# Optimization experiments

Hardware: AMD Instinct MI355X
Metric: run time of the kernel (lower is better)

The kernel has to match this reference:

```python
import jax, jax.numpy as jnp
import numpy as np

FEAT_SIZE, HIDDEN_SIZE, ATT_SIZE = 2048, 1024, 512
BATCH, FEAT_NUM = 64, 512


def setup_inputs() -> dict:
    key = jax.random.key(0)
    ks = jax.random.split(key, 8)
    s = lambda fan_in: 1.0 / np.sqrt(fan_in)
    return {
        "feats": jax.random.normal(ks[0], (BATCH, FEAT_NUM, FEAT_SIZE), jnp.float32),
        "key": jax.random.normal(ks[1], (BATCH, HIDDEN_SIZE), jnp.float32),
        "wh_w": jax.random.uniform(ks[2], (ATT_SIZE, HIDDEN_SIZE), jnp.float32, -s(HIDDEN_SIZE), s(HIDDEN_SIZE)),
        "wh_b": jax.random.uniform(ks[3], (ATT_SIZE,), jnp.float32, -s(HIDDEN_SIZE), s(HIDDEN_SIZE)),
        "wv_w": jax.random.uniform(ks[4], (ATT_SIZE, FEAT_SIZE), jnp.float32, -s(FEAT_SIZE), s(FEAT_SIZE)),
        "wv_b": jax.random.uniform(ks[5], (ATT_SIZE,), jnp.float32, -s(FEAT_SIZE), s(FEAT_SIZE)),
        "wa_w": jax.random.uniform(ks[6], (1, ATT_SIZE), jnp.float32, -s(ATT_SIZE), s(ATT_SIZE)),
    }


def reference(feats, key, wh_w, wh_b, wv_w, wv_b, wa_w):
    # v = wv(feats): (B, N, A)
    v = jnp.einsum('bnf,af->bna', feats, wv_w) + wv_b
    # h = wh(key): (B, A), broadcast-added over feat_num
    h = key @ wh_w.T + wh_b
    inputs = h[:, None, :] + v                       # (B, N, A)
    scores = jnp.einsum('bna,a->bn', jnp.tanh(inputs), wa_w[0])  # (B, N)
    alpha = jax.nn.softmax(scores, axis=1)           # (B, N)
    att_feats = jnp.einsum('bn,bnf->bf', alpha, feats)  # (B, F)
    return (att_feats, alpha)
```

## Files before the change

### kernel.cpp

```cpp
#include <hip/hip_runtime.h>
#include <hip/hip_bf16.h>

#define FEATSZ 2048
#define HIDSZ  1024
#define ATTSZ  512
#define BATCH  64
#define FEATN  512

typedef float  f32x4  __attribute__((ext_vector_type(4)));
typedef __bf16 bf16x8 __attribute__((ext_vector_type(8)));

__device__ __forceinline__ unsigned short f2bf(float f) {
    union { float f; unsigned int u; } x; x.f = f;
    unsigned int u = x.u;
    return (unsigned short)((u + 0x7fffu + ((u >> 16) & 1u)) >> 16);
}

__global__ void k_h(const float* __restrict__ key, const float* __restrict__ wh_w,
                    const float* __restrict__ wh_b, float* __restrict__ h) {
    const int b = blockIdx.y;
    const int ac = blockIdx.x;
    const int t = threadIdx.x;
    const int lane = t & 63, wv = t >> 6;
    float k16[16];
    const float* kb = key + b * HIDSZ;
#pragma unroll
    for (int j = 0; j < 16; ++j) k16[j] = kb[lane + 64 * j];
#pragma unroll 1
    for (int i = 0; i < 16; ++i) {
        int a = ac * 64 + wv * 16 + i;
        const float* wr = wh_w + (size_t)a * HIDSZ;
        float s = 0.f;
#pragma unroll
        for (int j = 0; j < 16; ++j) s += k16[j] * wr[lane + 64 * j];
#pragma unroll
        for (int d = 32; d; d >>= 1) s += __shfl_xor(s, d);
        if (lane == 0) h[b * ATTSZ + a] = s + wh_b[a];
    }
}

__global__ void k_wvcvt(const float* __restrict__ wv_w, unsigned short* __restrict__ wvb) {
    int idx = blockIdx.x * 256 + threadIdx.x;
    int a = idx >> 11, k = idx & 2047;
    int CF = a >> 4, c = a & 15, ks = k >> 5, kin = k & 31;
    int lane = c + ((kin >> 3) << 4);
    int dst = ((ks * 32 + CF) * 64 + lane) * 8 + (kin & 7);
    wvb[dst] = f2bf(wv_w[idx]);
}

__global__ __launch_bounds__(512) void k_scores(
        const float* __restrict__ feats, const unsigned short* __restrict__ wvb,
        const float* __restrict__ h, const float* __restrict__ wv_b,
        const float* __restrict__ wa, float* __restrict__ scores) {
    __shared__ __align__(16) char Abuf[4][8192];
    __shared__ float scp[8][128];
    const int t = threadIdx.x, lane = t & 63, w = t >> 6;
    const int m0 = blockIdx.x * 128, b = blockIdx.x >> 2;

    const int srow = t >> 2, sq = t & 3;
    const float* gsrc = feats + (size_t)(m0 + srow) * FEATSZ + sq * 8;
    const int wboff = srow * 64 + ((sq ^ ((t >> 3) & 3)) * 16);

    const int rbase = (lane & 15) * 64 + (((lane >> 4) ^ ((lane >> 1) & 3)) * 16);

    const unsigned short* wb = wvb + (size_t)(w * 4) * 512 + lane * 8;

    f32x4 acc[8][4];
#pragma unroll
    for (int m = 0; m < 8; ++m)
#pragma unroll
        for (int cf = 0; cf < 4; ++cf) acc[m][cf] = (f32x4)0.0f;

    f32x4 GA0, GA1, GB0, GB1;
    bf16x8 BX[4], BY[4];

    auto loadBX = [&](int tile) {
#pragma unroll
        for (int cf = 0; cf < 4; ++cf) BX[cf] = *(const bf16x8*)(wb + (size_t)(tile * 32 + cf) * 512);
    };
    auto loadBY = [&](int tile) {
#pragma unroll
        for (int cf = 0; cf < 4; ++cf) BY[cf] = *(const bf16x8*)(wb + (size_t)(tile * 32 + cf) * 512);
    };
    auto writeA = [&](f32x4 r0, f32x4 r1, int tile) {
        bf16x8 v;
        v[0] = (__bf16)r0[0]; v[1] = (__bf16)r0[1]; v[2] = (__bf16)r0[2]; v[3] = (__bf16)r0[3];
        v[4] = (__bf16)r1[0]; v[5] = (__bf16)r1[1]; v[6] = (__bf16)r1[2]; v[7] = (__bf16)r1[3];
        *(bf16x8*)__builtin_assume_aligned(&Abuf[tile & 3][0] + wboff, 16) = v;
    };
    auto bar = [&]() {
        asm volatile("s_waitcnt lgkmcnt(0)" ::: "memory");
        __builtin_amdgcn_s_barrier();
        __builtin_amdgcn_sched_barrier(0);
    };

    {
        const float* p0 = gsrc;
        GA0 = *(const f32x4*)p0;        GA1 = *(const f32x4*)(p0 + 4);
        const float* p1 = gsrc + 32;
        GB0 = *(const f32x4*)p1;        GB1 = *(const f32x4*)(p1 + 4);
        loadBX(0);
        writeA(GA0, GA1, 0);
        bar();
    }

#pragma unroll 1
    for (int jj = 0; jj < 32; ++jj) {
        const int j = jj * 2;
        if (j <= 61) {
            const float* p = gsrc + (j + 2) * 32;
            GA0 = *(const f32x4*)p; GA1 = *(const f32x4*)(p + 4);
        }
        loadBY(j + 1);
        writeA(GB0, GB1, j + 1);
        {
            const char* ab = &Abuf[j & 3][0];
            __builtin_amdgcn_s_setprio(1);
#pragma unroll
            for (int m = 0; m < 8; ++m) {
                bf16x8 a = *(const bf16x8*)__builtin_assume_aligned(ab + m * 1024 + rbase, 16);
#pragma unroll
                for (int cf = 0; cf < 4; ++cf)
                    acc[m][cf] = __builtin_amdgcn_mfma_f32_16x16x32_bf16(a, BX[cf], acc[m][cf], 0, 0, 0);
            }
            __builtin_amdgcn_s_setprio(0);
        }
        bar();
        const int j1 = j + 1;
        if (j1 <= 61) {
            const float* p = gsrc + (j1 + 2) * 32;
            GB0 = *(const f32x4*)p; GB1 = *(const f32x4*)(p + 4);
        }
        if (j1 <= 62) loadBX(j1 + 1);
        if (j1 <= 62) writeA(GA0, GA1, j1 + 1);
        {
            const char* ab = &Abuf[j1 & 3][0];
            __builtin_amdgcn_s_setprio(1);
#pragma unroll
            for (int m = 0; m < 8; ++m) {
                bf16x8 a = *(const bf16x8*)__builtin_assume_aligned(ab + m * 1024 + rbase, 16);
#pragma unroll
                for (int cf = 0; cf < 4; ++cf)
                    acc[m][cf] = __builtin_amdgcn_mfma_f32_16x16x32_bf16(a, BY[cf], acc[m][cf], 0, 0, 0);
            }
            __builtin_amdgcn_s_setprio(0);
        }
        bar();
    }

    const int c16 = lane & 15, q4 = lane >> 4;
    float hreg[4], wreg[4];
#pragma unroll
    for (int cf = 0; cf < 4; ++cf) {
        int a = w * 64 + cf * 16 + c16;
        hreg[cf] = h[b * ATTSZ + a] + wv_b[a];
        wreg[cf] = wa[a];
    }
    float pv[8][4];
#pragma unroll
    for (int m = 0; m < 8; ++m)
#pragma unroll
        for (int jr = 0; jr < 4; ++jr) pv[m][jr] = 0.f;
#pragma unroll
    for (int m = 0; m < 8; ++m)
#pragma unroll
        for (int cf = 0; cf < 4; ++cf)
#pragma unroll
            for (int jr = 0; jr < 4; ++jr)
                pv[m][jr] += tanhf(acc[m][cf][jr] + hreg[cf]) * wreg[cf];
#pragma unroll
    for (int m = 0; m < 8; ++m)
#pragma unroll
        for (int jr = 0; jr < 4; ++jr) {
            float v = pv[m][jr];
            v += __shfl_xor(v, 1); v += __shfl_xor(v, 2);
            v += __shfl_xor(v, 4); v += __shfl_xor(v, 8);
            pv[m][jr] = v;
        }
    if (c16 == 0) {
#pragma unroll
        for (int m = 0; m < 8; ++m)
#pragma unroll
            for (int jr = 0; jr < 4; ++jr)
                scp[w][m * 16 + q4 * 4 + jr] = pv[m][jr];
    }
    __syncthreads();
    if (t < 128) {
        float s = 0.f;
#pragma unroll
        for (int ww = 0; ww < 8; ++ww) s += scp[ww][t];
        scores[m0 + t] = s;
    }
}

__global__ void k_softmax(const float* __restrict__ scores, float* __restrict__ alpha) {
    __shared__ float red[16];
    const int b = blockIdx.x, t = threadIdx.x;
    const int lane = t & 63, w = t >> 6;
    float s = scores[b * FEATN + t];
    float m = s;
#pragma unroll
    for (int d = 32; d; d >>= 1) m = fmaxf(m, __shfl_xor(m, d));
    if (lane == 0) red[w] = m;
    __syncthreads();
    if (t == 0) {
        float mm = red[0];
        for (int i = 1; i < 8; ++i) mm = fmaxf(mm, red[i]);
        red[8] = mm;
    }
    __syncthreads();
    float e = __expf(s - red[8]);
    float sum = e;
#pragma unroll
    for (int d = 32; d; d >>= 1) sum += __shfl_xor(sum, d);
    if (lane == 0) red[w] = sum;
    __syncthreads();
    if (t == 0) {
        float ss = 0.f;
        for (int i = 0; i < 8; ++i) ss += red[i];
        red[9] = 1.0f / ss;
    }
    __syncthreads();
    alpha[b * FEATN + t] = e * red[9];
}

__global__ void k_att_part(const float* __restrict__ feats, const float* __restrict__ alpha,
                           float* __restrict__ part) {
    const int b = blockIdx.x, fc = blockIdx.y, ns = blockIdx.z, t = threadIdx.x;
    const int f0 = fc * 1024 + t * 4;
    const float* fp = feats + (size_t)(b * FEATN + ns * 128) * FEATSZ + f0;
    const float* al = alpha + b * FEATN + ns * 128;
    float4 acc = {0.f, 0.f, 0.f, 0.f};
#pragma unroll 4
    for (int i = 0; i < 128; ++i) {
        float a = al[i];
        float4 v = *(const float4*)(fp + (size_t)i * FEATSZ);
        acc.x += a * v.x; acc.y += a * v.y; acc.z += a * v.z; acc.w += a * v.w;
    }
    *(float4*)(part + ((size_t)ns * BATCH + b) * FEATSZ + f0) = acc;
}

__global__ void k_att_red(const float* __restrict__ part, float* __restrict__ out) {
    const int idx = (blockIdx.x * 256 + threadIdx.x) * 4;
    float4 s = *(const float4*)(part + idx);
#pragma unroll
    for (int z = 1; z < 4; ++z) {
        float4 v = *(const float4*)(part + (size_t)z * (BATCH * FEATSZ) + idx);
        s.x += v.x; s.y += v.y; s.z += v.z; s.w += v.w;
    }
    *(float4*)(out + idx) = s;
}

extern "C" void kernel_launch(void* const* d_in, const int* in_sizes, int n_in,
                              void* d_out, int out_size, void* d_ws, size_t ws_size,
                              hipStream_t stream) {
    const float* feats = (const float*)d_in[0];
    const float* key   = (const float*)d_in[1];
    const float* wh_w  = (const float*)d_in[2];
    const float* wh_b  = (const float*)d_in[3];
    const float* wv_w  = (const float*)d_in[4];
    const float* wv_b  = (const float*)d_in[5];
    const float* wa_w  = (const float*)d_in[6];

    float* out_att   = (float*)d_out;
    float* out_alpha = out_att + BATCH * FEATSZ;

    char* ws = (char*)d_ws;
    float* h            = (float*)(ws);
    float* scores       = (float*)(ws + 131072);
    unsigned short* wvb = (unsigned short*)(ws + 262144);
    float* part         = (float*)(ws + 262144);

    hipLaunchKernelGGL(k_h,        dim3(8, 64),    dim3(256), 0, stream, key, wh_w, wh_b, h);
    hipLaunchKernelGGL(k_wvcvt,    dim3(4096),     dim3(256), 0, stream, wv_w, wvb);
    hipLaunchKernelGGL(k_scores,   dim3(256),      dim3(512), 0, stream, feats, wvb, h, wv_b, wa_w, scores);
    hipLaunchKernelGGL(k_softmax,  dim3(64),       dim3(512), 0, stream, scores, out_alpha);
    hipLaunchKernelGGL(k_att_part, dim3(64, 2, 4), dim3(256), 0, stream, feats, out_alpha, part);
    hipLaunchKernelGGL(k_att_red,  dim3(128),      dim3(256), 0, stream, part, out_att);
}
```

Baseline: 161.0 us.

## Retile scores GEMM to 256-row by 256-column blocks with split-N partial scores

The scores kernel now has each block cover 256 feature rows and half of the 512 attention columns, instead of 128 rows and all columns. It uses 64-wide K tiles double-buffered in 64KB of LDS with an XOR swizzle and interleaves global loads, conversion and MFMA phases. The two column halves write partial scores that the softmax kernel sums. The goal is better reuse of the feats tile per weight load and more overlap of loads with MFMA, at the cost of much more LDS per block, lower occupancy and an extra partial-score buffer.

```diff
diff --git a/kernel.cpp b/kernel.cpp
--- a/kernel.cpp
+++ b/kernel.cpp
@@ -51,19 +51,21 @@
 __global__ __launch_bounds__(512) void k_scores(
         const float* __restrict__ feats, const unsigned short* __restrict__ wvb,
         const float* __restrict__ h, const float* __restrict__ wv_b,
-        const float* __restrict__ wa, float* __restrict__ scores) {
-    __shared__ __align__(16) char Abuf[4][8192];
-    __shared__ float scp[8][128];
+        const float* __restrict__ wa, float* __restrict__ part_sc) {
+    __shared__ __align__(16) char Abuf[2][32768];
+    __shared__ float scp[4][256];
     const int t = threadIdx.x, lane = t & 63, w = t >> 6;
-    const int m0 = blockIdx.x * 128, b = blockIdx.x >> 2;
-
-    const int srow = t >> 2, sq = t & 3;
-    const float* gsrc = feats + (size_t)(m0 + srow) * FEATSZ + sq * 8;
-    const int wboff = srow * 64 + ((sq ^ ((t >> 3) & 3)) * 16);
-
-    const int rbase = (lane & 15) * 64 + (((lane >> 4) ^ ((lane >> 1) & 3)) * 16);
-
-    const unsigned short* wb = wvb + (size_t)(w * 4) * 512 + lane * 8;
+    const int wm = w >> 2, wn = w & 3;
+    const int mb = blockIdx.x >> 1, nt = blockIdx.x & 1;
+    const int m0 = mb * 256, b = blockIdx.x >> 2;
+
+    const float* gbase = feats + (size_t)(m0 + (t >> 3)) * FEATSZ + (t & 7) * 8;
+    const int woff = ((t >> 3) * 128) + ((((t & 7) ^ ((t >> 3) & 7))) * 16);
+
+    const unsigned short* wbase = wvb + (size_t)(nt * 16 + wn * 4) * 512 + lane * 8;
+
+    const int arow = wm * 128 + (lane & 15);
+    const int aq = lane >> 4, ax = lane & 7;
 
     f32x4 acc[8][4];
 #pragma unroll
@@ -71,88 +73,82 @@
 #pragma unroll
         for (int cf = 0; cf < 4; ++cf) acc[m][cf] = (f32x4)0.0f;
 
-    f32x4 GA0, GA1, GB0, GB1;
-    bf16x8 BX[4], BY[4];
-
-    auto loadBX = [&](int tile) {
-#pragma unroll
-        for (int cf = 0; cf < 4; ++cf) BX[cf] = *(const bf16x8*)(wb + (size_t)(tile * 32 + cf) * 512);
-    };
-    auto loadBY = [&](int tile) {
-#pragma unroll
-        for (int cf = 0; cf < 4; ++cf) BY[cf] = *(const bf16x8*)(wb + (size_t)(tile * 32 + cf) * 512);
-    };
-    auto writeA = [&](f32x4 r0, f32x4 r1, int tile) {
+    bf16x8 BA[4], BB[4];
+    f32x4 G0a, G0b, G1a, G1b, G2a, G2b, G3a, G3b;
+
+    auto issueG = [&](int kt, int p, f32x4& ga, f32x4& gb) {
+        const float* s = gbase + (size_t)p * (64 * FEATSZ) + kt * 64;
+        ga = *(const f32x4*)s;
+        gb = *(const f32x4*)(s + 4);
+    };
+    auto loadB = [&](bf16x8(&B)[4], int kkg) {
+#pragma unroll
+        for (int cf = 0; cf < 4; ++cf)
+            B[cf] = *(const bf16x8*)(wbase + (size_t)(kkg * 32 + cf) * 512);
+    };
+    auto cvtWrite = [&](char* bw, int p, f32x4 ga, f32x4 gb) {
         bf16x8 v;
-        v[0] = (__bf16)r0[0]; v[1] = (__bf16)r0[1]; v[2] = (__bf16)r0[2]; v[3] = (__bf16)r0[3];
-        v[4] = (__bf16)r1[0]; v[5] = (__bf16)r1[1]; v[6] = (__bf16)r1[2]; v[7] = (__bf16)r1[3];
-        *(bf16x8*)__builtin_assume_aligned(&Abuf[tile & 3][0] + wboff, 16) = v;
-    };
-    auto bar = [&]() {
+        v[0] = (__bf16)ga[0]; v[1] = (__bf16)ga[1]; v[2] = (__bf16)ga[2]; v[3] = (__bf16)ga[3];
+        v[4] = (__bf16)gb[0]; v[5] = (__bf16)gb[1]; v[6] = (__bf16)gb[2]; v[7] = (__bf16)gb[3];
+        *(bf16x8*)__builtin_assume_aligned(bw + p * 8192 + woff, 16) = v;
+    };
+    auto mfmaPhase = [&](const char* br, int mg, int kk, bf16x8(&B)[4]) {
+        bf16x8 a0 = *(const bf16x8*)__builtin_assume_aligned(br + (arow + (mg + 0) * 16) * 128 + (((kk * 4 + aq) ^ ax) * 16), 16);
+        bf16x8 a1 = *(const bf16x8*)__builtin_assume_aligned(br + (arow + (mg + 1) * 16) * 128 + (((kk * 4 + aq) ^ ax) * 16), 16);
+        bf16x8 a2 = *(const bf16x8*)__builtin_assume_aligned(br + (arow + (mg + 2) * 16) * 128 + (((kk * 4 + aq) ^ ax) * 16), 16);
+        bf16x8 a3 = *(const bf16x8*)__builtin_assume_aligned(br + (arow + (mg + 3) * 16) * 128 + (((kk * 4 + aq) ^ ax) * 16), 16);
+        __builtin_amdgcn_s_setprio(1);
+#pragma unroll
+        for (int cf = 0; cf < 4; ++cf) acc[mg + 0][cf] = __builtin_amdgcn_mfma_f32_16x16x32_bf16(a0, B[cf], acc[mg + 0][cf], 0, 0, 0);
+#pragma unroll
+        for (int cf = 0; cf < 4; ++cf) acc[mg + 1][cf] = __builtin_amdgcn_mfma_f32_16x16x32_bf16(a1, B[cf], acc[mg + 1][cf], 0, 0, 0);
+#pragma unroll
+        for (int cf = 0; cf < 4; ++cf) acc[mg + 2][cf] = __builtin_amdgcn_mfma_f32_16x16x32_bf16(a2, B[cf], acc[mg + 2][cf], 0, 0, 0);
+#pragma unroll
+        for (int cf = 0; cf < 4; ++cf) acc[mg + 3][cf] = __builtin_amdgcn_mfma_f32_16x16x32_bf16(a3, B[cf], acc[mg + 3][cf], 0, 0, 0);
+        __builtin_amdgcn_s_setprio(0);
+        __builtin_amdgcn_sched_barrier(0);
+    };
+
+    issueG(0, 0, G0a, G0b); issueG(0, 1, G1a, G1b);
+    issueG(0, 2, G2a, G2b); issueG(0, 3, G3a, G3b);
+    loadB(BA, 0);
+    cvtWrite(&Abuf[0][0], 0, G0a, G0b);
+    cvtWrite(&Abuf[0][0], 1, G1a, G1b);
+    cvtWrite(&Abuf[0][0], 2, G2a, G2b);
+    cvtWrite(&Abuf[0][0], 3, G3a, G3b);
+    issueG(1, 0, G0a, G0b); issueG(1, 1, G1a, G1b);
+    issueG(1, 2, G2a, G2b); issueG(1, 3, G3a, G3b);
+    __syncthreads();
+
+#pragma unroll 1
+    for (int kt = 0; kt < 32; ++kt) {
+        const char* br = &Abuf[kt & 1][0];
+        char* bw = &Abuf[(kt & 1) ^ 1][0];
+        loadB(BB, kt * 2 + 1);
+        if (kt < 31) cvtWrite(bw, 0, G0a, G0b);
+        if (kt < 30) issueG(kt + 2, 0, G0a, G0b);
+        mfmaPhase(br, 0, 0, BA);
+        if (kt < 31) cvtWrite(bw, 1, G1a, G1b);
+        if (kt < 30) issueG(kt + 2, 1, G1a, G1b);
+        mfmaPhase(br, 4, 0, BA);
+        if (kt < 31) loadB(BA, (kt + 1) * 2);
+        if (kt < 31) cvtWrite(bw, 2, G2a, G2b);
+        if (kt < 30) issueG(kt + 2, 2, G2a, G2b);
+        mfmaPhase(br, 0, 1, BB);
+        if (kt < 31) cvtWrite(bw, 3, G3a, G3b);
+        if (kt < 30) issueG(kt + 2, 3, G3a, G3b);
+        mfmaPhase(br, 4, 1, BB);
         asm volatile("s_waitcnt lgkmcnt(0)" ::: "memory");
         __builtin_amdgcn_s_barrier();
         __builtin_amdgcn_sched_barrier(0);
-    };
-
-    {
-        const float* p0 = gsrc;
-        GA0 = *(const f32x4*)p0;        GA1 = *(const f32x4*)(p0 + 4);
-        const float* p1 = gsrc + 32;
-        GB0 = *(const f32x4*)p1;        GB1 = *(const f32x4*)(p1 + 4);
-        loadBX(0);
-        writeA(GA0, GA1, 0);
-        bar();
-    }
-
-#pragma unroll 1
-    for (int jj = 0; jj < 32; ++jj) {
-        const int j = jj * 2;
-        if (j <= 61) {
-            const float* p = gsrc + (j + 2) * 32;
-            GA0 = *(const f32x4*)p; GA1 = *(const f32x4*)(p + 4);
-        }
-        loadBY(j + 1);
-        writeA(GB0, GB1, j + 1);
-        {
-            const char* ab = &Abuf[j & 3][0];
-            __builtin_amdgcn_s_setprio(1);
-#pragma unroll
-            for (int m = 0; m < 8; ++m) {
-                bf16x8 a = *(const bf16x8*)__builtin_assume_aligned(ab + m * 1024 + rbase, 16);
-#pragma unroll
-                for (int cf = 0; cf < 4; ++cf)
-                    acc[m][cf] = __builtin_amdgcn_mfma_f32_16x16x32_bf16(a, BX[cf], acc[m][cf], 0, 0, 0);
-            }
-            __builtin_amdgcn_s_setprio(0);
-        }
-        bar();
-        const int j1 = j + 1;
-        if (j1 <= 61) {
-            const float* p = gsrc + (j1 + 2) * 32;
-            GB0 = *(const f32x4*)p; GB1 = *(const f32x4*)(p + 4);
-        }
-        if (j1 <= 62) loadBX(j1 + 1);
-        if (j1 <= 62) writeA(GA0, GA1, j1 + 1);
-        {
-            const char* ab = &Abuf[j1 & 3][0];
-            __builtin_amdgcn_s_setprio(1);
-#pragma unroll
-            for (int m = 0; m < 8; ++m) {
-                bf16x8 a = *(const bf16x8*)__builtin_assume_aligned(ab + m * 1024 + rbase, 16);
-#pragma unroll
-                for (int cf = 0; cf < 4; ++cf)
-                    acc[m][cf] = __builtin_amdgcn_mfma_f32_16x16x32_bf16(a, BY[cf], acc[m][cf], 0, 0, 0);
-            }
-            __builtin_amdgcn_s_setprio(0);
-        }
-        bar();
     }
 
     const int c16 = lane & 15, q4 = lane >> 4;
     float hreg[4], wreg[4];
 #pragma unroll
     for (int cf = 0; cf < 4; ++cf) {
-        int a = w * 64 + cf * 16 + c16;
+        int a = nt * 256 + wn * 64 + cf * 16 + c16;
         hreg[cf] = h[b * ATTSZ + a] + wv_b[a];
         wreg[cf] = wa[a];
     }
@@ -182,22 +178,20 @@
         for (int m = 0; m < 8; ++m)
 #pragma unroll
             for (int jr = 0; jr < 4; ++jr)
-                scp[w][m * 16 + q4 * 4 + jr] = pv[m][jr];
-    }
-    __syncthreads();
-    if (t < 128) {
-        float s = 0.f;
-#pragma unroll
-        for (int ww = 0; ww < 8; ++ww) s += scp[ww][t];
-        scores[m0 + t] = s;
-    }
-}
-
-__global__ void k_softmax(const float* __restrict__ scores, float* __restrict__ alpha) {
+                scp[wn][wm * 128 + m * 16 + q4 * 4 + jr] = pv[m][jr];
+    }
+    __syncthreads();
+    if (t < 256)
+        part_sc[nt * (BATCH * FEATN) + m0 + t]
+            = scp[0][t] + scp[1][t] + scp[2][t] + scp[3][t];
+}
+
+__global__ void k_softmax(const float* __restrict__ part_sc, float* __restrict__ alpha) {
     __shared__ float red[16];
     const int b = blockIdx.x, t = threadIdx.x;
     const int lane = t & 63, w = t >> 6;
-    float s = scores[b * FEATN + t];
+    const int r = b * FEATN + t;
+    float s = part_sc[r] + part_sc[BATCH * FEATN + r];
     float m = s;
 #pragma unroll
     for (int d = 32; d; d >>= 1) m = fmaxf(m, __shfl_xor(m, d));
@@ -267,14 +261,14 @@
 
     char* ws = (char*)d_ws;
     float* h            = (float*)(ws);
-    float* scores       = (float*)(ws + 131072);
-    unsigned short* wvb = (unsigned short*)(ws + 262144);
-    float* part         = (float*)(ws + 262144);
+    float* part_sc      = (float*)(ws + 131072);
+    unsigned short* wvb = (unsigned short*)(ws + 393216);
+    float* part         = (float*)(ws + 393216);
 
     hipLaunchKernelGGL(k_h,        dim3(8, 64),    dim3(256), 0, stream, key, wh_w, wh_b, h);
     hipLaunchKernelGGL(k_wvcvt,    dim3(4096),     dim3(256), 0, stream, wv_w, wvb);
-    hipLaunchKernelGGL(k_scores,   dim3(256),      dim3(512), 0, stream, feats, wvb, h, wv_b, wa_w, scores);
-    hipLaunchKernelGGL(k_softmax,  dim3(64),       dim3(512), 0, stream, scores, out_alpha);
+    hipLaunchKernelGGL(k_scores,   dim3(256),      dim3(512), 0, stream, feats, wvb, h, wv_b, wa_w, part_sc);
+    hipLaunchKernelGGL(k_softmax,  dim3(64),       dim3(512), 0, stream, part_sc, out_alpha);
     hipLaunchKernelGGL(k_att_part, dim3(64, 2, 4), dim3(256), 0, stream, feats, out_alpha, part);
     hipLaunchKernelGGL(k_att_red,  dim3(128),      dim3(256), 0, stream, part, out_att);
 }
```

After: 165.5 us. 2.8% more time.

## Halve k_scores M-tile to 64 rows and double-buffer A tile

Applied to the files above, without the earlier changes.

Shrinks each k_scores block from 128 to 64 feature rows, doubles the grid to 512 blocks and requests 4 blocks per SM via launch bounds. The A-tile staging drops from a 4-deep to a 2-deep LDS ring with one-tile lookahead, and only half the threads stage the feats tile. The aim is more blocks across the CUs and lower register and LDS pressure per block for better occupancy and latency hiding. In exchange the wv weight tiles are reloaded twice as often per row, and each K-step does less MFMA work to hide its global load.

```diff
diff --git a/kernel.cpp b/kernel.cpp
--- a/kernel.cpp
+++ b/kernel.cpp
@@ -48,45 +48,63 @@
     wvb[dst] = f2bf(wv_w[idx]);
 }
 
-__global__ __launch_bounds__(512) void k_scores(
+__global__ __launch_bounds__(512, 4) void k_scores(
         const float* __restrict__ feats, const unsigned short* __restrict__ wvb,
         const float* __restrict__ h, const float* __restrict__ wv_b,
         const float* __restrict__ wa, float* __restrict__ scores) {
-    __shared__ __align__(16) char Abuf[4][8192];
-    __shared__ float scp[8][128];
+    __shared__ __align__(16) char Abuf[2][4096];
+    __shared__ float scp[8][64];
     const int t = threadIdx.x, lane = t & 63, w = t >> 6;
-    const int m0 = blockIdx.x * 128, b = blockIdx.x >> 2;
+    const int m0 = blockIdx.x * 64, b = blockIdx.x >> 3;
 
     const int srow = t >> 2, sq = t & 3;
     const float* gsrc = feats + (size_t)(m0 + srow) * FEATSZ + sq * 8;
-    const int wboff = srow * 64 + ((sq ^ ((t >> 3) & 3)) * 16);
-
-    const int rbase = (lane & 15) * 64 + (((lane >> 4) ^ ((lane >> 1) & 3)) * 16);
+    const int wboff = srow * 64 + ((sq ^ ((srow >> 1) & 3)) * 16);
+    const bool stager = (t < 256);
+
+    const int rbase = (lane & 15) * 64 + (((lane >> 4) ^ (((lane & 15) >> 1) & 3)) * 16);
 
     const unsigned short* wb = wvb + (size_t)(w * 4) * 512 + lane * 8;
 
-    f32x4 acc[8][4];
-#pragma unroll
-    for (int m = 0; m < 8; ++m)
+    f32x4 acc[4][4];
+#pragma unroll
+    for (int m = 0; m < 4; ++m)
 #pragma unroll
         for (int cf = 0; cf < 4; ++cf) acc[m][cf] = (f32x4)0.0f;
 
-    f32x4 GA0, GA1, GB0, GB1;
     bf16x8 BX[4], BY[4];
-
-    auto loadBX = [&](int tile) {
-#pragma unroll
-        for (int cf = 0; cf < 4; ++cf) BX[cf] = *(const bf16x8*)(wb + (size_t)(tile * 32 + cf) * 512);
-    };
-    auto loadBY = [&](int tile) {
-#pragma unroll
-        for (int cf = 0; cf < 4; ++cf) BY[cf] = *(const bf16x8*)(wb + (size_t)(tile * 32 + cf) * 512);
-    };
-    auto writeA = [&](f32x4 r0, f32x4 r1, int tile) {
-        bf16x8 v;
-        v[0] = (__bf16)r0[0]; v[1] = (__bf16)r0[1]; v[2] = (__bf16)r0[2]; v[3] = (__bf16)r0[3];
-        v[4] = (__bf16)r1[0]; v[5] = (__bf16)r1[1]; v[6] = (__bf16)r1[2]; v[7] = (__bf16)r1[3];
-        *(bf16x8*)__builtin_assume_aligned(&Abuf[tile & 3][0] + wboff, 16) = v;
+    auto loadBX = [&](int kk) {
+#pragma unroll
+        for (int cf = 0; cf < 4; ++cf) BX[cf] = *(const bf16x8*)(wb + (size_t)(kk * 32 + cf) * 512);
+    };
+    auto loadBY = [&](int kk) {
+#pragma unroll
+        for (int cf = 0; cf < 4; ++cf) BY[cf] = *(const bf16x8*)(wb + (size_t)(kk * 32 + cf) * 512);
+    };
+    auto cvtWrite = [&](int buf, f32x4 u0, f32x4 u1) {
+        if (stager) {
+            bf16x8 v;
+            v[0] = (__bf16)u0[0]; v[1] = (__bf16)u0[1]; v[2] = (__bf16)u0[2]; v[3] = (__bf16)u0[3];
+            v[4] = (__bf16)u1[0]; v[5] = (__bf16)u1[1]; v[6] = (__bf16)u1[2]; v[7] = (__bf16)u1[3];
+            *(bf16x8*)__builtin_assume_aligned(&Abuf[buf][0] + wboff, 16) = v;
+        }
+    };
+    auto mfma16 = [&](int buf, bf16x8(&B)[4]) {
+        const char* ab = &Abuf[buf][0];
+        bf16x8 a0 = *(const bf16x8*)__builtin_assume_aligned(ab + 0 * 1024 + rbase, 16);
+        bf16x8 a1 = *(const bf16x8*)__builtin_assume_aligned(ab + 1 * 1024 + rbase, 16);
+        bf16x8 a2 = *(const bf16x8*)__builtin_assume_aligned(ab + 2 * 1024 + rbase, 16);
+        bf16x8 a3 = *(const bf16x8*)__builtin_assume_aligned(ab + 3 * 1024 + rbase, 16);
+        __builtin_amdgcn_s_setprio(1);
+#pragma unroll
+        for (int cf = 0; cf < 4; ++cf) acc[0][cf] = __builtin_amdgcn_mfma_f32_16x16x32_bf16(a0, B[cf], acc[0][cf], 0, 0, 0);
+#pragma unroll
+        for (int cf = 0; cf < 4; ++cf) acc[1][cf] = __builtin_amdgcn_mfma_f32_16x16x32_bf16(a1, B[cf], acc[1][cf], 0, 0, 0);
+#pragma unroll
+        for (int cf = 0; cf < 4; ++cf) acc[2][cf] = __builtin_amdgcn_mfma_f32_16x16x32_bf16(a2, B[cf], acc[2][cf], 0, 0, 0);
+#pragma unroll
+        for (int cf = 0; cf < 4; ++cf) acc[3][cf] = __builtin_amdgcn_mfma_f32_16x16x32_bf16(a3, B[cf], acc[3][cf], 0, 0, 0);
+        __builtin_amdgcn_s_setprio(0);
     };
     auto bar = [&]() {
         asm volatile("s_waitcnt lgkmcnt(0)" ::: "memory");
@@ -95,57 +113,41 @@
     };
 
     {
-        const float* p0 = gsrc;
-        GA0 = *(const f32x4*)p0;        GA1 = *(const f32x4*)(p0 + 4);
-        const float* p1 = gsrc + 32;
-        GB0 = *(const f32x4*)p1;        GB1 = *(const f32x4*)(p1 + 4);
+        f32x4 u0, u1;
+        if (stager) {
+            u0 = *(const f32x4*)gsrc;
+            u1 = *(const f32x4*)(gsrc + 4);
+        }
         loadBX(0);
-        writeA(GA0, GA1, 0);
+        cvtWrite(0, u0, u1);
         bar();
     }
 
 #pragma unroll 1
     for (int jj = 0; jj < 32; ++jj) {
         const int j = jj * 2;
-        if (j <= 61) {
-            const float* p = gsrc + (j + 2) * 32;
-            GA0 = *(const f32x4*)p; GA1 = *(const f32x4*)(p + 4);
-        }
-        loadBY(j + 1);
-        writeA(GB0, GB1, j + 1);
         {
-            const char* ab = &Abuf[j & 3][0];
-            __builtin_amdgcn_s_setprio(1);
-#pragma unroll
-            for (int m = 0; m < 8; ++m) {
-                bf16x8 a = *(const bf16x8*)__builtin_assume_aligned(ab + m * 1024 + rbase, 16);
-#pragma unroll
-                for (int cf = 0; cf < 4; ++cf)
-                    acc[m][cf] = __builtin_amdgcn_mfma_f32_16x16x32_bf16(a, BX[cf], acc[m][cf], 0, 0, 0);
+            f32x4 u0, u1;
+            if (stager && j < 63) {
+                const float* p = gsrc + (j + 1) * 32;
+                u0 = *(const f32x4*)p; u1 = *(const f32x4*)(p + 4);
             }
-            __builtin_amdgcn_s_setprio(0);
-        }
-        bar();
-        const int j1 = j + 1;
-        if (j1 <= 61) {
-            const float* p = gsrc + (j1 + 2) * 32;
-            GB0 = *(const f32x4*)p; GB1 = *(const f32x4*)(p + 4);
-        }
-        if (j1 <= 62) loadBX(j1 + 1);
-        if (j1 <= 62) writeA(GA0, GA1, j1 + 1);
+            if (j < 63) loadBY(j + 1);
+            mfma16(0, BX);
+            if (j < 63) cvtWrite(1, u0, u1);
+            bar();
+        }
         {
-            const char* ab = &Abuf[j1 & 3][0];
-            __builtin_amdgcn_s_setprio(1);
-#pragma unroll
-            for (int m = 0; m < 8; ++m) {
-                bf16x8 a = *(const bf16x8*)__builtin_assume_aligned(ab + m * 1024 + rbase, 16);
-#pragma unroll
-                for (int cf = 0; cf < 4; ++cf)
-                    acc[m][cf] = __builtin_amdgcn_mfma_f32_16x16x32_bf16(a, BY[cf], acc[m][cf], 0, 0, 0);
+            f32x4 u0, u1;
+            if (stager && j < 62) {
+                const float* p = gsrc + (j + 2) * 32;
+                u0 = *(const f32x4*)p; u1 = *(const f32x4*)(p + 4);
             }
-            __builtin_amdgcn_s_setprio(0);
-        }
-        bar();
+            if (j < 62) loadBX(j + 2);
+            mfma16(1, BY);
+            if (j < 62) cvtWrite(0, u0, u1);
+            bar();
+        }
     }
 
     const int c16 = lane & 15, q4 = lane >> 4;
@@ -156,20 +158,20 @@
         hreg[cf] = h[b * ATTSZ + a] + wv_b[a];
         wreg[cf] = wa[a];
     }
-    float pv[8][4];
-#pragma unroll
-    for (int m = 0; m < 8; ++m)
+    float pv[4][4];
+#pragma unroll
+    for (int m = 0; m < 4; ++m)
 #pragma unroll
         for (int jr = 0; jr < 4; ++jr) pv[m][jr] = 0.f;
 #pragma unroll
-    for (int m = 0; m < 8; ++m)
+    for (int m = 0; m < 4; ++m)
 #pragma unroll
         for (int cf = 0; cf < 4; ++cf)
 #pragma unroll
             for (int jr = 0; jr < 4; ++jr)
                 pv[m][jr] += tanhf(acc[m][cf][jr] + hreg[cf]) * wreg[cf];
 #pragma unroll
-    for (int m = 0; m < 8; ++m)
+    for (int m = 0; m < 4; ++m)
 #pragma unroll
         for (int jr = 0; jr < 4; ++jr) {
             float v = pv[m][jr];
@@ -179,13 +181,13 @@
         }
     if (c16 == 0) {
 #pragma unroll
-        for (int m = 0; m < 8; ++m)
+        for (int m = 0; m < 4; ++m)
 #pragma unroll
             for (int jr = 0; jr < 4; ++jr)
                 scp[w][m * 16 + q4 * 4 + jr] = pv[m][jr];
     }
     __syncthreads();
-    if (t < 128) {
+    if (t < 64) {
         float s = 0.f;
 #pragma unroll
         for (int ww = 0; ww < 8; ++ww) s += scp[ww][t];
@@ -273,7 +275,7 @@
 
     hipLaunchKernelGGL(k_h,        dim3(8, 64),    dim3(256), 0, stream, key, wh_w, wh_b, h);
     hipLaunchKernelGGL(k_wvcvt,    dim3(4096),     dim3(256), 0, stream, wv_w, wvb);
-    hipLaunchKernelGGL(k_scores,   dim3(256),      dim3(512), 0, stream, feats, wvb, h, wv_b, wa_w, scores);
+    hipLaunchKernelGGL(k_scores,   dim3(512),      dim3(512), 0, stream, feats, wvb, h, wv_b, wa_w, scores);
     hipLaunchKernelGGL(k_softmax,  dim3(64),       dim3(512), 0, stream, scores, out_alpha);
     hipLaunchKernelGGL(k_att_part, dim3(64, 2, 4), dim3(256), 0, stream, feats, out_alpha, part);
     hipLaunchKernelGGL(k_att_red,  dim3(128),      dim3(256), 0, stream, part, out_att);
```

Result: slower. 213.8 us (+32.8%).
